# Performance work log

Hardware: AMD Instinct MI355X
Metric: run time of the kernel (lower is better)

Reference implementation:

```python
import jax, jax.numpy as jnp
import numpy as np

N = 100000      # nodes
E = 1600000     # edges (avg degree 16)
D_IN, D_H1, D_H2, D_OUT = 512, 256, 256, 64


def setup_inputs() -> dict:
    key = jax.random.key(0)
    ks = jax.random.split(key, 8)
    x = jax.random.normal(ks[0], (N, D_IN), dtype=jnp.float32)
    row = jax.random.randint(ks[1], (E,), 0, N, dtype=jnp.int32)
    col = jax.random.randint(ks[2], (E,), 0, N, dtype=jnp.int32)
    vals = jax.random.uniform(ks[3], (E,), dtype=jnp.float32)
    # xavier-normal-ish scaling for weights
    W1 = jax.random.normal(ks[4], (D_IN, D_H1), dtype=jnp.float32) * np.sqrt(2.0 / (D_IN + D_H1))
    W2 = jax.random.normal(ks[5], (D_H1, D_H2), dtype=jnp.float32) * np.sqrt(2.0 / (D_H1 + D_H2))
    W3 = jax.random.normal(ks[6], (D_H2, D_OUT), dtype=jnp.float32) * np.sqrt(2.0 / (D_H2 + D_OUT))
    b1 = jnp.zeros((D_H1,), dtype=jnp.float32)
    b2 = jnp.zeros((D_H2,), dtype=jnp.float32)
    b3 = jnp.zeros((D_OUT,), dtype=jnp.float32)
    return {"x": x, "row": row, "col": col, "vals": vals,
            "W1": W1, "b1": b1, "W2": W2, "b2": b2, "W3": W3, "b3": b3}


def reference(x, row, col, vals, W1, b1, W2, b2, W3, b3):
    n = x.shape[0]

    def spmm(h):
        # out[i] = sum_{e: row[e]==i} vals[e] * h[col[e]]  (COO spmm)
        return jax.ops.segment_sum(vals[:, None] * h[col], row, num_segments=n)

    # layer 1: linear -> spmm -> relu  (dropout p=0 -> identity)
    h = jax.nn.relu(spmm(x @ W1 + b1))
    # layer 2
    h = jax.nn.relu(spmm(h @ W2 + b2))
    # output layer: no activation, no dropout
    return spmm(h @ W3 + b3)
```

## Files before the change

kernel.cpp:

```cpp
#include <hip/hip_runtime.h>

typedef _Float16 f16;
typedef _Float16 f16x4 __attribute__((ext_vector_type(4)));
typedef _Float16 f16x8 __attribute__((ext_vector_type(8)));
typedef float f32x4 __attribute__((ext_vector_type(4)));

#define DEVI __device__ __forceinline__

static constexpr int CAP = 64;

DEVI void g2l16(const void* g, void* l) {
  __builtin_amdgcn_global_load_lds(
      (const __attribute__((address_space(1))) void*)g,
      (__attribute__((address_space(3))) void*)l, 16, 0, 0);
}

DEVI f16x8 cvt8(float4 a, float4 b) {
  f16x8 r;
  r[0] = (f16)a.x; r[1] = (f16)a.y; r[2] = (f16)a.z; r[3] = (f16)a.w;
  r[4] = (f16)b.x; r[5] = (f16)b.y; r[6] = (f16)b.z; r[7] = (f16)b.w;
  return r;
}

__global__ __launch_bounds__(256)
void prep_w(const float* __restrict__ W1, const float* __restrict__ W2,
            const float* __restrict__ W3, f16* __restrict__ WT1,
            f16* __restrict__ WT2, f16* __restrict__ WT3) {
  int t = blockIdx.x * 256 + threadIdx.x;
  if (t < 131072) {
    int n = t >> 9, k = t & 511;
    WT1[t] = (f16)W1[k * 256 + n];
  } else if (t < 131072 + 65536) {
    int u = t - 131072; int n = u >> 8, k = u & 255;
    WT2[u] = (f16)W2[k * 256 + n];
  } else if (t < 131072 + 65536 + 16384) {
    int u = t - 131072 - 65536; int n = u >> 8, k = u & 255;
    WT3[u] = (f16)W3[k * 64 + n];
  }
}

__global__ __launch_bounds__(256)
void build_slots(const int* __restrict__ row, const int* __restrict__ col,
                 const float* __restrict__ vals, int* __restrict__ cnt,
                 int2* __restrict__ slots, int E) {
  int e = blockIdx.x * 256 + threadIdx.x;
  if (e >= E) return;
  int r = row[e];
  int p = atomicAdd(&cnt[r], 1);
  if (p < CAP) slots[(size_t)r * CAP + p] = make_int2(col[e], __float_as_int(vals[e]));
}

template <int BN, bool AF32>
__global__ __launch_bounds__(256)
void gemm_kern(const void* __restrict__ Ap, const f16* __restrict__ WT,
               const float* __restrict__ bias, f16* __restrict__ C,
               int M, int K, int N) {
  constexpr int BM = 128;
  constexpr int NT = BN / 32;
  __shared__ f16 As[BM * 32];
  __shared__ f16 Bs[BN * 32];

  const int tid = threadIdx.x;
  const int wave = tid >> 6, lane = tid & 63;
  const int wm = wave >> 1, wn = wave & 1;
  const int quad = lane >> 4, l16 = lane & 15;
  const int bm = blockIdx.x, bn = blockIdx.y;
  const int r0 = bm * BM;

  f32x4 acc[4][NT];
#pragma unroll
  for (int mt = 0; mt < 4; ++mt)
#pragma unroll
    for (int nt = 0; nt < NT; ++nt) {
      f32x4 z = {0.f, 0.f, 0.f, 0.f};
      acc[mt][nt] = z;
    }

  const int kiters = K >> 5;
  for (int kb = 0; kb < kiters; ++kb) {
    if constexpr (AF32) {
      const float* Af = (const float*)Ap;
      int row = r0 + (tid >> 1);
      row = min(row, M - 1);
      const int half = tid & 1;
      const float4* gp = (const float4*)(Af + (size_t)row * K + kb * 32 + half * 16);
      float4 v0 = gp[0], v1 = gp[1], v2 = gp[2], v3 = gp[3];
      f16x8* dst = (f16x8*)&As[(tid >> 1) * 32 + half * 16];
      dst[0] = cvt8(v0, v1);
      dst[1] = cvt8(v2, v3);
    } else {
      const f16* Ah = (const f16*)Ap;
#pragma unroll
      for (int t = 0; t < 2; ++t) {
        int inst = wave * 2 + t;
        int row = r0 + inst * 16 + (lane >> 2);
        row = min(row, M - 1);
        const f16* gp = Ah + (size_t)row * K + kb * 32 + (lane & 3) * 8;
        g2l16(gp, &As[inst * 16 * 32]);
      }
    }
#pragma unroll
    for (int t = 0; t < BN / 64; ++t) {
      int inst = wave * (BN / 64) + t;
      int n = bn * BN + inst * 16 + (lane >> 2);
      const f16* gp = WT + (size_t)n * K + kb * 32 + (lane & 3) * 8;
      g2l16(gp, &Bs[inst * 16 * 32]);
    }
    __syncthreads();

    f16x8 af[4], bf[NT];
#pragma unroll
    for (int mt = 0; mt < 4; ++mt)
      af[mt] = *(const f16x8*)&As[(wm * 64 + mt * 16 + l16) * 32 + quad * 8];
#pragma unroll
    for (int nt = 0; nt < NT; ++nt)
      bf[nt] = *(const f16x8*)&Bs[(wn * (BN / 2) + nt * 16 + l16) * 32 + quad * 8];
#pragma unroll
    for (int mt = 0; mt < 4; ++mt)
#pragma unroll
      for (int nt = 0; nt < NT; ++nt)
        acc[mt][nt] = __builtin_amdgcn_mfma_f32_16x16x32_f16(af[mt], bf[nt], acc[mt][nt], 0, 0, 0);
    __syncthreads();
  }

  float bv[NT];
#pragma unroll
  for (int nt = 0; nt < NT; ++nt)
    bv[nt] = bias[bn * BN + wn * (BN / 2) + nt * 16 + l16];
#pragma unroll
  for (int mt = 0; mt < 4; ++mt) {
#pragma unroll
    for (int nt = 0; nt < NT; ++nt) {
      int colg = bn * BN + wn * (BN / 2) + nt * 16 + l16;
#pragma unroll
      for (int r = 0; r < 4; ++r) {
        int grow = r0 + wm * 64 + mt * 16 + quad * 4 + r;
        if (grow < M)
          C[(size_t)grow * N + colg] = (f16)(acc[mt][nt][r] + bv[nt]);
      }
    }
  }
}

__global__ __launch_bounds__(256)
void spmm_relu256(const f16* __restrict__ T, const int2* __restrict__ slots,
                  const int* __restrict__ cnt, f16* __restrict__ H, int nrows) {
  const int wave = threadIdx.x >> 6, lane = threadIdx.x & 63;
  const int i = blockIdx.x * 4 + wave;
  if (i >= nrows) return;
  const int c = min(cnt[i], CAP);
  const int2* sl = slots + (size_t)i * CAP;
  float a0 = 0.f, a1 = 0.f, a2 = 0.f, a3 = 0.f;
  int j = 0;
  for (; j + 4 <= c; j += 4) {
    int2 e0 = sl[j], e1 = sl[j + 1], e2 = sl[j + 2], e3 = sl[j + 3];
    f16x4 u0 = ((const f16x4*)(T + (size_t)e0.x * 256))[lane];
    f16x4 u1 = ((const f16x4*)(T + (size_t)e1.x * 256))[lane];
    f16x4 u2 = ((const f16x4*)(T + (size_t)e2.x * 256))[lane];
    f16x4 u3 = ((const f16x4*)(T + (size_t)e3.x * 256))[lane];
    float v0 = __int_as_float(e0.y), v1 = __int_as_float(e1.y);
    float v2 = __int_as_float(e2.y), v3 = __int_as_float(e3.y);
    a0 += v0 * (float)u0.x + v1 * (float)u1.x + v2 * (float)u2.x + v3 * (float)u3.x;
    a1 += v0 * (float)u0.y + v1 * (float)u1.y + v2 * (float)u2.y + v3 * (float)u3.y;
    a2 += v0 * (float)u0.z + v1 * (float)u1.z + v2 * (float)u2.z + v3 * (float)u3.z;
    a3 += v0 * (float)u0.w + v1 * (float)u1.w + v2 * (float)u2.w + v3 * (float)u3.w;
  }
  for (; j < c; ++j) {
    int2 e = sl[j];
    f16x4 u = ((const f16x4*)(T + (size_t)e.x * 256))[lane];
    float v = __int_as_float(e.y);
    a0 += v * (float)u.x; a1 += v * (float)u.y;
    a2 += v * (float)u.z; a3 += v * (float)u.w;
  }
  f16x4 o;
  o.x = (f16)fmaxf(a0, 0.f); o.y = (f16)fmaxf(a1, 0.f);
  o.z = (f16)fmaxf(a2, 0.f); o.w = (f16)fmaxf(a3, 0.f);
  ((f16x4*)(H + (size_t)i * 256))[lane] = o;
}

__global__ __launch_bounds__(256)
void spmm_out64(const f16* __restrict__ T, const int2* __restrict__ slots,
                const int* __restrict__ cnt, float* __restrict__ out, int nrows) {
  const int wave = threadIdx.x >> 6, lane = threadIdx.x & 63;
  const int i = blockIdx.x * 4 + wave;
  if (i >= nrows) return;
  const int c = min(cnt[i], CAP);
  const int2* sl = slots + (size_t)i * CAP;
  float a = 0.f;
  int j = 0;
  for (; j + 4 <= c; j += 4) {
    int2 e0 = sl[j], e1 = sl[j + 1], e2 = sl[j + 2], e3 = sl[j + 3];
    float u0 = (float)T[(size_t)e0.x * 64 + lane];
    float u1 = (float)T[(size_t)e1.x * 64 + lane];
    float u2 = (float)T[(size_t)e2.x * 64 + lane];
    float u3 = (float)T[(size_t)e3.x * 64 + lane];
    a += __int_as_float(e0.y) * u0 + __int_as_float(e1.y) * u1
       + __int_as_float(e2.y) * u2 + __int_as_float(e3.y) * u3;
  }
  for (; j < c; ++j) {
    int2 e = sl[j];
    a += __int_as_float(e.y) * (float)T[(size_t)e.x * 64 + lane];
  }
  out[(size_t)i * 64 + lane] = a;
}

extern "C" void kernel_launch(void* const* d_in, const int* in_sizes, int n_in,
                              void* d_out, int out_size, void* d_ws, size_t ws_size,
                              hipStream_t stream) {
  const float* x    = (const float*)d_in[0];
  const int*   row  = (const int*)d_in[1];
  const int*   col  = (const int*)d_in[2];
  const float* vals = (const float*)d_in[3];
  const float* W1   = (const float*)d_in[4];
  const float* b1   = (const float*)d_in[5];
  const float* W2   = (const float*)d_in[6];
  const float* b2   = (const float*)d_in[7];
  const float* W3   = (const float*)d_in[8];
  const float* b3   = (const float*)d_in[9];
  float* out = (float*)d_out;

  const int N = in_sizes[0] / 512;
  const int E = in_sizes[1];

  char* ws = (char*)d_ws;
  const size_t MiB = 1ull << 20;
  int*  cnt   = (int*)ws;
  int2* slots = (int2*)(ws + 1 * MiB);
  f16*  WT1   = (f16*)(ws + 52 * MiB);
  f16*  WT2   = WT1 + 256 * 512;
  f16*  WT3   = WT2 + 256 * 256;
  f16*  T     = (f16*)(ws + 53 * MiB);
  f16*  H     = (f16*)(ws + 104 * MiB);

  hipMemsetAsync(cnt, 0, (size_t)N * sizeof(int), stream);
  prep_w<<<(131072 + 65536 + 16384 + 255) / 256, 256, 0, stream>>>(W1, W2, W3, WT1, WT2, WT3);
  build_slots<<<(E + 255) / 256, 256, 0, stream>>>(row, col, vals, cnt, slots, E);

  dim3 g12((N + 127) / 128, 2);
  dim3 g3((N + 127) / 128, 1);
  dim3 gs((N + 3) / 4);

  gemm_kern<128, true><<<g12, 256, 0, stream>>>(x, WT1, b1, T, N, 512, 256);
  spmm_relu256<<<gs, 256, 0, stream>>>(T, slots, cnt, H, N);
  gemm_kern<128, false><<<g12, 256, 0, stream>>>(H, WT2, b2, T, N, 256, 256);
  spmm_relu256<<<gs, 256, 0, stream>>>(T, slots, cnt, H, N);
  gemm_kern<64, false><<<g3, 256, 0, stream>>>(H, WT3, b3, T, N, 256, 64);
  spmm_out64<<<gs, 256, 0, stream>>>(T, slots, cnt, out, N);
}
```

Measured before the change: 827.7 us.

## Double-buffer GEMM LDS tiles and pre-swizzle weights into MFMA fragment order

```diff
diff --git a/kernel.cpp b/kernel.cpp
--- a/kernel.cpp
+++ b/kernel.cpp
@@ -27,16 +27,24 @@
             const float* __restrict__ W3, f16* __restrict__ WT1,
             f16* __restrict__ WT2, f16* __restrict__ WT3) {
   int t = blockIdx.x * 256 + threadIdx.x;
-  if (t < 131072) {
-    int n = t >> 9, k = t & 511;
-    WT1[t] = (f16)W1[k * 256 + n];
-  } else if (t < 131072 + 65536) {
-    int u = t - 131072; int n = u >> 8, k = u & 255;
-    WT2[u] = (f16)W2[k * 256 + n];
-  } else if (t < 131072 + 65536 + 16384) {
-    int u = t - 131072 - 65536; int n = u >> 8, k = u & 255;
-    WT3[u] = (f16)W3[k * 64 + n];
-  }
+  const float* W; f16* O; int N; int u;
+  if (t < 16384) {
+    W = W1; O = WT1; N = 256; u = t;
+  } else if (t < 16384 + 8192) {
+    W = W2; O = WT2; N = 256; u = t - 16384;
+  } else if (t < 16384 + 8192 + 2048) {
+    W = W3; O = WT3; N = 64;  u = t - 24576;
+  } else return;
+  const int per = (N >> 4) * 64;
+  const int kc = u / per;
+  const int rem = u - kc * per;
+  const int l = rem & 63;
+  const int n = ((rem >> 6) << 4) + (l & 15);
+  const int kb = kc * 32 + ((l >> 4) << 3);
+  f16x8 o;
+#pragma unroll
+  for (int j = 0; j < 8; ++j) o[j] = (f16)W[(size_t)(kb + j) * N + n];
+  *(f16x8*)(O + (size_t)u * 8) = o;
 }
 
 __global__ __launch_bounds__(256)
@@ -57,8 +65,10 @@
                int M, int K, int N) {
   constexpr int BM = 128;
   constexpr int NT = BN / 32;
-  __shared__ f16 As[BM * 32];
-  __shared__ f16 Bs[BN * 32];
+  constexpr int BFRAGS = BN / 16;
+  constexpr int BSHOTS = BN / 64;
+  __shared__ f16 As[2][BM * 32];
+  __shared__ f16 Bs[2][BN * 32];
 
   const int tid = threadIdx.x;
   const int wave = tid >> 6, lane = tid & 63;
@@ -66,6 +76,8 @@
   const int quad = lane >> 4, l16 = lane & 15;
   const int bm = blockIdx.x, bn = blockIdx.y;
   const int r0 = bm * BM;
+  const int kiters = K >> 5;
+  const int nfrag16 = N >> 4;
 
   f32x4 acc[4][NT];
 #pragma unroll
@@ -76,51 +88,101 @@
       acc[mt][nt] = z;
     }
 
-  const int kiters = K >> 5;
-  for (int kb = 0; kb < kiters; ++kb) {
+  {
+#pragma unroll
+    for (int s = 0; s < BSHOTS; ++s) {
+      int i16 = s * 256 + tid;
+      const f16* gp = WT + (((size_t)bn * BFRAGS) * 64 + i16) * 8;
+      g2l16(gp, &Bs[0][(s * 256 + wave * 64) * 8]);
+    }
     if constexpr (AF32) {
       const float* Af = (const float*)Ap;
-      int row = r0 + (tid >> 1);
-      row = min(row, M - 1);
-      const int half = tid & 1;
-      const float4* gp = (const float4*)(Af + (size_t)row * K + kb * 32 + half * 16);
-      float4 v0 = gp[0], v1 = gp[1], v2 = gp[2], v3 = gp[3];
-      f16x8* dst = (f16x8*)&As[(tid >> 1) * 32 + half * 16];
-      dst[0] = cvt8(v0, v1);
-      dst[1] = cvt8(v2, v3);
+#pragma unroll
+      for (int s = 0; s < 2; ++s) {
+        int i16 = s * 256 + tid;
+        int g = i16 >> 6, la = i16 & 63;
+        int row = min(r0 + g * 16 + (la & 15), M - 1);
+        const float4* gp = (const float4*)(Af + (size_t)row * K + ((la >> 4) << 3));
+        float4 v0 = gp[0], v1 = gp[1];
+        *(f16x8*)&As[0][i16 * 8] = cvt8(v0, v1);
+      }
     } else {
       const f16* Ah = (const f16*)Ap;
 #pragma unroll
-      for (int t = 0; t < 2; ++t) {
-        int inst = wave * 2 + t;
-        int row = r0 + inst * 16 + (lane >> 2);
-        row = min(row, M - 1);
-        const f16* gp = Ah + (size_t)row * K + kb * 32 + (lane & 3) * 8;
-        g2l16(gp, &As[inst * 16 * 32]);
-      }
-    }
-#pragma unroll
-    for (int t = 0; t < BN / 64; ++t) {
-      int inst = wave * (BN / 64) + t;
-      int n = bn * BN + inst * 16 + (lane >> 2);
-      const f16* gp = WT + (size_t)n * K + kb * 32 + (lane & 3) * 8;
-      g2l16(gp, &Bs[inst * 16 * 32]);
-    }
-    __syncthreads();
+      for (int s = 0; s < 2; ++s) {
+        int i16 = s * 256 + tid;
+        int g = i16 >> 6, la = i16 & 63;
+        int row = min(r0 + g * 16 + (la & 15), M - 1);
+        const f16* gp = Ah + (size_t)row * K + ((la >> 4) << 3);
+        g2l16(gp, &As[0][(s * 256 + wave * 64) * 8]);
+      }
+    }
+  }
+  __syncthreads();
+
+  int c = 0;
+  for (int kb = 0; kb < kiters; ++kb) {
+    const bool more = (kb + 1) < kiters;
+    float4 ra00, ra01, ra10, ra11;
+
+    if (more) {
+      const int kn = kb + 1;
+#pragma unroll
+      for (int s = 0; s < BSHOTS; ++s) {
+        int i16 = s * 256 + tid;
+        const f16* gp = WT + (((size_t)kn * nfrag16 + (size_t)bn * BFRAGS) * 64 + i16) * 8;
+        g2l16(gp, &Bs[c ^ 1][(s * 256 + wave * 64) * 8]);
+      }
+      if constexpr (AF32) {
+        const float* Af = (const float*)Ap;
+        {
+          int i16 = tid;
+          int g = i16 >> 6, la = i16 & 63;
+          int row = min(r0 + g * 16 + (la & 15), M - 1);
+          const float4* gp = (const float4*)(Af + (size_t)row * K + kn * 32 + ((la >> 4) << 3));
+          ra00 = gp[0]; ra01 = gp[1];
+        }
+        {
+          int i16 = 256 + tid;
+          int g = i16 >> 6, la = i16 & 63;
+          int row = min(r0 + g * 16 + (la & 15), M - 1);
+          const float4* gp = (const float4*)(Af + (size_t)row * K + kn * 32 + ((la >> 4) << 3));
+          ra10 = gp[0]; ra11 = gp[1];
+        }
+      } else {
+        const f16* Ah = (const f16*)Ap;
+#pragma unroll
+        for (int s = 0; s < 2; ++s) {
+          int i16 = s * 256 + tid;
+          int g = i16 >> 6, la = i16 & 63;
+          int row = min(r0 + g * 16 + (la & 15), M - 1);
+          const f16* gp = Ah + (size_t)row * K + kn * 32 + ((la >> 4) << 3);
+          g2l16(gp, &As[c ^ 1][(s * 256 + wave * 64) * 8]);
+        }
+      }
+    }
 
     f16x8 af[4], bf[NT];
 #pragma unroll
     for (int mt = 0; mt < 4; ++mt)
-      af[mt] = *(const f16x8*)&As[(wm * 64 + mt * 16 + l16) * 32 + quad * 8];
+      af[mt] = *(const f16x8*)&As[c][((wm * 4 + mt) * 64 + lane) * 8];
 #pragma unroll
     for (int nt = 0; nt < NT; ++nt)
-      bf[nt] = *(const f16x8*)&Bs[(wn * (BN / 2) + nt * 16 + l16) * 32 + quad * 8];
+      bf[nt] = *(const f16x8*)&Bs[c][((wn * NT + nt) * 64 + lane) * 8];
 #pragma unroll
     for (int mt = 0; mt < 4; ++mt)
 #pragma unroll
       for (int nt = 0; nt < NT; ++nt)
         acc[mt][nt] = __builtin_amdgcn_mfma_f32_16x16x32_f16(af[mt], bf[nt], acc[mt][nt], 0, 0, 0);
+
+    if constexpr (AF32) {
+      if (more) {
+        *(f16x8*)&As[c ^ 1][tid * 8] = cvt8(ra00, ra01);
+        *(f16x8*)&As[c ^ 1][(256 + tid) * 8] = cvt8(ra10, ra11);
+      }
+    }
     __syncthreads();
+    c ^= 1;
   }
 
   float bv[NT];
@@ -233,7 +295,7 @@
   f16*  H     = (f16*)(ws + 104 * MiB);
 
   hipMemsetAsync(cnt, 0, (size_t)N * sizeof(int), stream);
-  prep_w<<<(131072 + 65536 + 16384 + 255) / 256, 256, 0, stream>>>(W1, W2, W3, WT1, WT2, WT3);
+  prep_w<<<(16384 + 8192 + 2048 + 255) / 256, 256, 0, stream>>>(W1, W2, W3, WT1, WT2, WT3);
   build_slots<<<(E + 255) / 256, 256, 0, stream>>>(row, col, vals, cnt, slots, E);
 
   dim3 g12((N + 127) / 128, 2);
```

New measurement: 842.8 us. Within noise of the previous version (+1.8%).

## Pre-swizzle weights into MFMA fragment layout and load GEMM operands directly

Applied to the files above, without the earlier changes.

```diff
diff --git a/kernel.cpp b/kernel.cpp
--- a/kernel.cpp
+++ b/kernel.cpp
@@ -8,12 +8,6 @@
 #define DEVI __device__ __forceinline__
 
 static constexpr int CAP = 64;
-
-DEVI void g2l16(const void* g, void* l) {
-  __builtin_amdgcn_global_load_lds(
-      (const __attribute__((address_space(1))) void*)g,
-      (__attribute__((address_space(3))) void*)l, 16, 0, 0);
-}
 
 DEVI f16x8 cvt8(float4 a, float4 b) {
   f16x8 r;
@@ -27,16 +21,24 @@
             const float* __restrict__ W3, f16* __restrict__ WT1,
             f16* __restrict__ WT2, f16* __restrict__ WT3) {
   int t = blockIdx.x * 256 + threadIdx.x;
-  if (t < 131072) {
-    int n = t >> 9, k = t & 511;
-    WT1[t] = (f16)W1[k * 256 + n];
-  } else if (t < 131072 + 65536) {
-    int u = t - 131072; int n = u >> 8, k = u & 255;
-    WT2[u] = (f16)W2[k * 256 + n];
-  } else if (t < 131072 + 65536 + 16384) {
-    int u = t - 131072 - 65536; int n = u >> 8, k = u & 255;
-    WT3[u] = (f16)W3[k * 64 + n];
-  }
+  const float* W; f16* O; int N; int u;
+  if (t < 16384) {
+    W = W1; O = WT1; N = 256; u = t;
+  } else if (t < 16384 + 8192) {
+    W = W2; O = WT2; N = 256; u = t - 16384;
+  } else if (t < 16384 + 8192 + 2048) {
+    W = W3; O = WT3; N = 64;  u = t - 24576;
+  } else return;
+  const int per = (N >> 4) * 64;
+  const int kc = u / per;
+  const int rem = u - kc * per;
+  const int l = rem & 63;
+  const int n = ((rem >> 6) << 4) + (l & 15);
+  const int kb = kc * 32 + ((l >> 4) << 3);
+  f16x8 o;
+#pragma unroll
+  for (int j = 0; j < 8; ++j) o[j] = (f16)W[(size_t)(kb + j) * N + n];
+  *(f16x8*)(O + (size_t)u * 8) = o;
 }
 
 __global__ __launch_bounds__(256)
@@ -50,91 +52,137 @@
   if (p < CAP) slots[(size_t)r * CAP + p] = make_int2(col[e], __float_as_int(vals[e]));
 }
 
-template <int BN, bool AF32>
-__global__ __launch_bounds__(256)
-void gemm_kern(const void* __restrict__ Ap, const f16* __restrict__ WT,
-               const float* __restrict__ bias, f16* __restrict__ C,
-               int M, int K, int N) {
-  constexpr int BM = 128;
-  constexpr int NT = BN / 32;
-  __shared__ f16 As[BM * 32];
-  __shared__ f16 Bs[BN * 32];
+__global__ __launch_bounds__(256)
+void gemm_l1(const float* __restrict__ A, const f16* __restrict__ WT,
+             const float* __restrict__ bias, f16* __restrict__ C, int M) {
+  constexpr int K = 512, N = 256, NF16 = N / 16;
+  __shared__ f16 As[64 * 256];
 
   const int tid = threadIdx.x;
   const int wave = tid >> 6, lane = tid & 63;
-  const int wm = wave >> 1, wn = wave & 1;
   const int quad = lane >> 4, l16 = lane & 15;
-  const int bm = blockIdx.x, bn = blockIdx.y;
-  const int r0 = bm * BM;
-
-  f32x4 acc[4][NT];
+  const int r0 = blockIdx.x * 64;
+
+  f32x4 acc[4][4];
 #pragma unroll
   for (int mt = 0; mt < 4; ++mt)
 #pragma unroll
-    for (int nt = 0; nt < NT; ++nt) {
+    for (int nt = 0; nt < 4; ++nt) {
       f32x4 z = {0.f, 0.f, 0.f, 0.f};
       acc[mt][nt] = z;
     }
 
-  const int kiters = K >> 5;
-  for (int kb = 0; kb < kiters; ++kb) {
-    if constexpr (AF32) {
-      const float* Af = (const float*)Ap;
-      int row = r0 + (tid >> 1);
-      row = min(row, M - 1);
-      const int half = tid & 1;
-      const float4* gp = (const float4*)(Af + (size_t)row * K + kb * 32 + half * 16);
-      float4 v0 = gp[0], v1 = gp[1], v2 = gp[2], v3 = gp[3];
-      f16x8* dst = (f16x8*)&As[(tid >> 1) * 32 + half * 16];
-      dst[0] = cvt8(v0, v1);
-      dst[1] = cvt8(v2, v3);
-    } else {
-      const f16* Ah = (const f16*)Ap;
-#pragma unroll
-      for (int t = 0; t < 2; ++t) {
-        int inst = wave * 2 + t;
-        int row = r0 + inst * 16 + (lane >> 2);
-        row = min(row, M - 1);
-        const f16* gp = Ah + (size_t)row * K + kb * 32 + (lane & 3) * 8;
-        g2l16(gp, &As[inst * 16 * 32]);
-      }
-    }
-#pragma unroll
-    for (int t = 0; t < BN / 64; ++t) {
-      int inst = wave * (BN / 64) + t;
-      int n = bn * BN + inst * 16 + (lane >> 2);
-      const f16* gp = WT + (size_t)n * K + kb * 32 + (lane & 3) * 8;
-      g2l16(gp, &Bs[inst * 16 * 32]);
+  for (int kc = 0; kc < 2; ++kc) {
+    if (kc) __syncthreads();
+#pragma unroll
+    for (int it = 0; it < 8; ++it) {
+      int i = it * 256 + tid;
+      int row = i >> 5, ko = i & 31;
+      int grow = min(r0 + row, M - 1);
+      const float4* gp = (const float4*)(A + (size_t)grow * K + kc * 256 + ko * 8);
+      float4 v0 = gp[0], v1 = gp[1];
+      int dst = (row * 512 + ko * 16) ^ ((row & 7) << 4);
+      *(f16x8*)((char*)As + dst) = cvt8(v0, v1);
     }
     __syncthreads();
-
-    f16x8 af[4], bf[NT];
+#pragma unroll
+    for (int kb = 0; kb < 8; ++kb) {
+      f16x8 af[4], bf[4];
+#pragma unroll
+      for (int mt = 0; mt < 4; ++mt) {
+        int row = mt * 16 + l16;
+        int src = (row * 512 + kb * 64 + quad * 16) ^ ((row & 7) << 4);
+        af[mt] = *(const f16x8*)((char*)As + src);
+      }
+      const int kg = kc * 8 + kb;
+#pragma unroll
+      for (int nt = 0; nt < 4; ++nt) {
+        int n16 = wave * 4 + nt;
+        bf[nt] = *(const f16x8*)(WT + ((size_t)(kg * NF16 + n16) * 64 + lane) * 8);
+      }
+#pragma unroll
+      for (int mt = 0; mt < 4; ++mt)
+#pragma unroll
+        for (int nt = 0; nt < 4; ++nt)
+          acc[mt][nt] = __builtin_amdgcn_mfma_f32_16x16x32_f16(af[mt], bf[nt], acc[mt][nt], 0, 0, 0);
+    }
+  }
+
+  float bv[4];
+#pragma unroll
+  for (int nt = 0; nt < 4; ++nt) bv[nt] = bias[wave * 64 + nt * 16 + l16];
+#pragma unroll
+  for (int mt = 0; mt < 4; ++mt) {
+#pragma unroll
+    for (int nt = 0; nt < 4; ++nt) {
+      int colg = wave * 64 + nt * 16 + l16;
+#pragma unroll
+      for (int r = 0; r < 4; ++r) {
+        int grow = r0 + mt * 16 + quad * 4 + r;
+        if (grow < M)
+          C[(size_t)grow * N + colg] = (f16)(acc[mt][nt][r] + bv[nt]);
+      }
+    }
+  }
+}
+
+template <int NTILES>
+__global__ __launch_bounds__(256)
+void gemm_direct(const f16* __restrict__ A, const f16* __restrict__ WT,
+                 const float* __restrict__ bias, f16* __restrict__ C, int M) {
+  constexpr int K = 256, N = NTILES * 64, NF16 = N / 16;
+  const int tid = threadIdx.x;
+  const int wave = tid >> 6, lane = tid & 63;
+  const int quad = lane >> 4, l16 = lane & 15;
+  const int gw = blockIdx.x * 4 + wave;
+  const int mtile = (NTILES == 1) ? gw : (gw / NTILES);
+  const int ntile = (NTILES == 1) ? 0 : (gw % NTILES);
+  const int r0 = mtile * 64;
+  if (r0 >= M) return;
+
+  size_t arow[4];
+#pragma unroll
+  for (int mt = 0; mt < 4; ++mt)
+    arow[mt] = (size_t)min(r0 + mt * 16 + l16, M - 1) * K;
+
+  f32x4 acc[4][4];
+#pragma unroll
+  for (int mt = 0; mt < 4; ++mt)
+#pragma unroll
+    for (int nt = 0; nt < 4; ++nt) {
+      f32x4 z = {0.f, 0.f, 0.f, 0.f};
+      acc[mt][nt] = z;
+    }
+
+#pragma unroll
+  for (int kb = 0; kb < 8; ++kb) {
+    f16x8 af[4], bf[4];
 #pragma unroll
     for (int mt = 0; mt < 4; ++mt)
-      af[mt] = *(const f16x8*)&As[(wm * 64 + mt * 16 + l16) * 32 + quad * 8];
-#pragma unroll
-    for (int nt = 0; nt < NT; ++nt)
-      bf[nt] = *(const f16x8*)&Bs[(wn * (BN / 2) + nt * 16 + l16) * 32 + quad * 8];
+      af[mt] = *(const f16x8*)(A + arow[mt] + kb * 32 + quad * 8);
+#pragma unroll
+    for (int nt = 0; nt < 4; ++nt) {
+      int n16 = ntile * 4 + nt;
+      bf[nt] = *(const f16x8*)(WT + ((size_t)(kb * NF16 + n16) * 64 + lane) * 8);
+    }
 #pragma unroll
     for (int mt = 0; mt < 4; ++mt)
 #pragma unroll
-      for (int nt = 0; nt < NT; ++nt)
+      for (int nt = 0; nt < 4; ++nt)
         acc[mt][nt] = __builtin_amdgcn_mfma_f32_16x16x32_f16(af[mt], bf[nt], acc[mt][nt], 0, 0, 0);
-    __syncthreads();
-  }
-
-  float bv[NT];
-#pragma unroll
-  for (int nt = 0; nt < NT; ++nt)
-    bv[nt] = bias[bn * BN + wn * (BN / 2) + nt * 16 + l16];
+  }
+
+  float bv[4];
+#pragma unroll
+  for (int nt = 0; nt < 4; ++nt) bv[nt] = bias[ntile * 64 + nt * 16 + l16];
 #pragma unroll
   for (int mt = 0; mt < 4; ++mt) {
 #pragma unroll
-    for (int nt = 0; nt < NT; ++nt) {
-      int colg = bn * BN + wn * (BN / 2) + nt * 16 + l16;
+    for (int nt = 0; nt < 4; ++nt) {
+      int colg = ntile * 64 + nt * 16 + l16;
 #pragma unroll
       for (int r = 0; r < 4; ++r) {
-        int grow = r0 + wm * 64 + mt * 16 + quad * 4 + r;
+        int grow = r0 + mt * 16 + quad * 4 + r;
         if (grow < M)
           C[(size_t)grow * N + colg] = (f16)(acc[mt][nt][r] + bv[nt]);
       }
@@ -233,17 +281,16 @@
   f16*  H     = (f16*)(ws + 104 * MiB);
 
   hipMemsetAsync(cnt, 0, (size_t)N * sizeof(int), stream);
-  prep_w<<<(131072 + 65536 + 16384 + 255) / 256, 256, 0, stream>>>(W1, W2, W3, WT1, WT2, WT3);
+  prep_w<<<(16384 + 8192 + 2048 + 255) / 256, 256, 0, stream>>>(W1, W2, W3, WT1, WT2, WT3);
   build_slots<<<(E + 255) / 256, 256, 0, stream>>>(row, col, vals, cnt, slots, E);
 
-  dim3 g12((N + 127) / 128, 2);
-  dim3 g3((N + 127) / 128, 1);
+  const int mt64 = (N + 63) / 64;
   dim3 gs((N + 3) / 4);
 
-  gemm_kern<128, true><<<g12, 256, 0, stream>>>(x, WT1, b1, T, N, 512, 256);
+  gemm_l1<<<mt64, 256, 0, stream>>>(x, WT1, b1, T, N);
   spmm_relu256<<<gs, 256, 0, stream>>>(T, slots, cnt, H, N);
-  gemm_kern<128, false><<<g12, 256, 0, stream>>>(H, WT2, b2, T, N, 256, 256);
+  gemm_direct<4><<<mt64, 256, 0, stream>>>(H, WT2, b2, T, N);
   spmm_relu256<<<gs, 256, 0, stream>>>(T, slots, cnt, H, N);
-  gemm_kern<64, false><<<g3, 256, 0, stream>>>(H, WT3, b3, T, N, 256, 64);
+  gemm_direct<1><<<(mt64 + 3) / 4, 256, 0, stream>>>(H, WT3, b3, T, N);
   spmm_out64<<<gs, 256, 0, stream>>>(T, slots, cnt, out, N);
 }
```

New measurement: 810.5 us. 1.02x faster.
